# Kernel tuning notes

Measured on AMD Instinct MI355X. Metric: run time of the kernel, lower is better.

## Reference

```python
import jax, jax.numpy as jnp
import numpy as np

DIM = 1024
HEADS = 16
DH = DIM // HEADS          # 64
SEQ_LEN = 4096
LATENT = 1024
HIST = SEQ_LEN - LATENT    # 3072
LN_EPS = 1e-5


def setup_inputs() -> dict:
    key = jax.random.key(0)
    ks = jax.random.split(key, 5)
    b = 2
    x = jax.random.normal(ks[0], (b, SEQ_LEN, DIM), dtype=jnp.float32)
    s = 0.02
    Wq = jax.random.normal(ks[1], (DIM, DIM), dtype=jnp.float32) * s
    Wkv = jax.random.normal(ks[2], (DIM, DIM), dtype=jnp.float32) * s
    Wo = jax.random.normal(ks[3], (DIM, DIM), dtype=jnp.float32) * s
    bo = jnp.zeros((DIM,), dtype=jnp.float32)
    gamma = jnp.ones((DH,), dtype=jnp.float32)
    beta = jnp.zeros((DH,), dtype=jnp.float32)
    return {"x": x, "Wq": Wq, "Wkv": Wkv, "Wo": Wo, "bo": bo,
            "gamma": gamma, "beta": beta}


def _rotate_half(t):
    t1, t2 = jnp.split(t, 2, axis=-1)
    return jnp.concatenate([-t2, t1], axis=-1)


def reference(x, Wq, Wkv, Wo, bo, gamma, beta):
    b, n, dim = x.shape
    # projections (nn.Linear: y = x @ W.T), split heads -> (b, h, n, d)
    q = jnp.einsum('bnd,ed->bne', x, Wq).reshape(b, n, HEADS, DH).transpose(0, 2, 1, 3)
    kv = jnp.einsum('bnd,ed->bne', x, Wkv).reshape(b, n, HEADS, DH).transpose(0, 2, 1, 3)

    # layer_num == 0: queries only for the latent segment
    q = q[:, :, HIST:, :]  # (b, h, latent, d)

    # rotary embeddings: concat-style freqs over head dim
    inv_freq = 1.0 / (10000.0 ** (jnp.arange(0, DH, 2, dtype=jnp.float32) / DH))
    freqs = jnp.arange(n, dtype=jnp.float32)[:, None] * inv_freq[None, :]  # (n, DH/2)
    emb = jnp.concatenate([freqs, freqs], axis=-1)  # (n, DH)
    cos, sin = jnp.cos(emb), jnp.sin(emb)
    q = q * cos[HIST:] + _rotate_half(q) * sin[HIST:]
    kv = kv * cos + _rotate_half(kv) * sin

    q = q * (DH ** -0.5)

    # per-kv LayerNorm over head dim
    mu = kv.mean(axis=-1, keepdims=True)
    var = ((kv - mu) ** 2).mean(axis=-1, keepdims=True)
    kvn = (kv - mu) * jax.lax.rsqrt(var + LN_EPS) * gamma + beta

    attn = jnp.einsum('bhid,bhjd->bhij', q, kvn)  # (b, h, latent, n)

    # causal mask only on latent columns: col j (>= HIST) masked if j-HIST > i
    i = jnp.arange(LATENT)[:, None]
    j = jnp.arange(n)[None, :]
    mask = (j - HIST) > i  # false for history columns (j < HIST)
    neg = -jnp.finfo(attn.dtype).max
    attn = jnp.where(mask, neg, attn)

    attn = jax.nn.softmax(attn, axis=-1)
    out = jnp.einsum('bhij,bhjd->bhid', attn, kvn)  # (b, h, latent, d)
    out = out.transpose(0, 2, 1, 3).reshape(b, LATENT, dim)
    return jnp.einsum('bnd,ed->bne', out, Wo) + bo
```

## Files before the change

kernel.cpp:

```cpp
#include <hip/hip_runtime.h>
#include <hip/hip_bf16.h>
#include <cstdint>

#define DIMC 1024
#define HEADS 16
#define DHH 64
#define SEQ 4096
#define LATENT 1024
#define HISTC 3072
#define BATCH 2

typedef __attribute__((ext_vector_type(8))) __bf16 bf16x8;
typedef __attribute__((ext_vector_type(4))) float f32x4;
typedef __attribute__((ext_vector_type(16))) float f32x16;

__global__ void k_prep(const float* __restrict__ x, const float* __restrict__ Wq,
                       const float* __restrict__ Wkv, const float* __restrict__ Wo,
                       __bf16* __restrict__ x16, __bf16* __restrict__ wq16,
                       __bf16* __restrict__ wkv16, __bf16* __restrict__ wo16,
                       float2* __restrict__ cs) {
  int bidx = blockIdx.x;
  if (bidx < 2048) {
    int base = bidx * 256 + threadIdx.x;
#pragma unroll
// ... 76 lines not shown

#pragma unroll
  for (int m = 0; m < 4; ++m)
#pragma unroll
    for (int n = 0; n < 4; ++n)
#pragma unroll
      for (int r = 0; r < 4; ++r) {
        int row = m0 + wr * 64 + m * 16 + (l >> 4) * 4 + r;
        int col = n0 + wc * 64 + n * 16 + (l & 15);
        float v = acc[m][n][r];
        if (BIAS) v += bias[col];
        C[(size_t)row * N + col] = v;
      }
}

__launch_bounds__(256)
__global__ void k_gemmqkv(const __bf16* __restrict__ x16,
                          const __bf16* __restrict__ wkv16,
                          const __bf16* __restrict__ wq16,
                          __bf16* __restrict__ kvn, __bf16* __restrict__ kvnT,
                          __bf16* __restrict__ qb,
                          const float* __restrict__ gamma,
                          const float* __restrict__ beta,
                          const float2* __restrict__ cstab) {
  __shared__ __align__(16) char lds[16384];
  const int t = threadIdx.x, l = t & 63, w = t >> 6;
  const int wr = w >> 1, wc = w & 1;
  const int by = blockIdx.x % 80;
  const bool isq = by >= 64;
  const int m0 = (isq ? (by - 64) : by) * 128;
  const int n0 = (blockIdx.x / 80) * 128;
  const __bf16* Bw = isq ? wq16 : wkv16;
  const int lrow = l & 15, lk = l >> 4;
  f32x4 acc[4][4] = {};

  for (int k0 = 0; k0 < 1024; k0 += 32) {
    if (k0) __syncthreads();
#pragma unroll
    for (int i = 0; i < 2; ++i) {
      int c = i * 256 + t;
      int row = c >> 2, kc = c & 3;
      int mi = m0 + row;
      if (isq) mi += HISTC + (mi >> 10) * HISTC;
      gload16(lds + c * 16, x16 + (size_t)mi * 1024 + k0 + kc * 8);
      gload16(lds + 8192 + c * 16, Bw + (size_t)(n0 + row) * 1024 + k0 + kc * 8);
    }
    __syncthreads();
    bf16x8 af[4], bfr[4];
#pragma unroll
    for (int m = 0; m < 4; ++m)
      af[m] = *reinterpret_cast<const bf16x8*>(lds + (wr * 64 + m * 16 + lrow) * 64 + lk * 16);
#pragma unroll
    for (int n = 0; n < 4; ++n)
      bfr[n] = *reinterpret_cast<const bf16x8*>(lds + 8192 + (wc * 64 + n * 16 + lrow) * 64 + lk * 16);
#pragma unroll
    for (int m = 0; m < 4; ++m)
#pragma unroll
      for (int n = 0; n < 4; ++n)
        acc[m][n] = __builtin_amdgcn_mfma_f32_16x16x32_bf16(af[m], bfr[n], acc[m][n], 0, 0, 0);
  }

#pragma unroll
  for (int m = 0; m < 4; ++m)
#pragma unroll
    for (int r = 0; r < 4; ++r) {
      int rl = wr * 64 + m * 16 + lk * 4 + r;
      int pos = isq ? (HISTC + ((m0 + rl) & 1023)) : ((m0 + rl) & 4095);
      float2 cs0 = cstab[pos * 32 + lrow];
      float2 cs1 = cstab[pos * 32 + 16 + lrow];
      float a0 = acc[m][0][r], a2 = acc[m][2][r];
      acc[m][0][r] = a0 * cs0.x - a2 * cs0.y;
      acc[m][2][r] = a2 * cs0.x + a0 * cs0.y;
      float a1 = acc[m][1][r], a3 = acc[m][3][r];
      acc[m][1][r] = a1 * cs1.x - a3 * cs1.y;
      acc[m][3][r] = a3 * cs1.x + a1 * cs1.y;
    }

  const int h = (n0 + wc * 64) >> 6;
  if (!isq) {
    float g4[4], b4[4];
#pragma unroll
    for (int n = 0; n < 4; ++n) { g4[n] = gamma[n * 16 + lrow]; b4[n] = beta[n * 16 + lrow]; }
#pragma unroll
    for (int m = 0; m < 4; ++m)
#pragma unroll
      for (int r = 0; r < 4; ++r) {
        float s1 = acc[m][0][r] + acc[m][1][r] + acc[m][2][r] + acc[m][3][r];
        float s2 = acc[m][0][r] * acc[m][0][r] + acc[m][1][r] * acc[m][1][r] +
                   acc[m][2][r] * acc[m][2][r] + acc[m][3][r] * acc[m][3][r];
#pragma unroll
        for (int mk = 1; mk < 16; mk <<= 1) {
          s1 += __shfl_xor(s1, mk);
          s2 += __shfl_xor(s2, mk);
        }
        float mu = s1 * 0.015625f;
        float var = s2 * 0.015625f - mu * mu;
        float inv = rsqrtf(var + 1e-5f);
#pragma unroll
        for (int n = 0; n < 4; ++n)
          acc[m][n][r] = (acc[m][n][r] - mu) * inv * g4[n] + b4[n];
      }
    const size_t hb = (size_t)((m0 >> 12) * HEADS + h);
#pragma unroll
    for (int m = 0; m < 4; ++m)
#pragma unroll
      for (int r = 0; r < 4; ++r) {
        int pos = (m0 + wr * 64 + m * 16 + lk * 4 + r) & 4095;
#pragma unroll
        for (int n = 0; n < 4; ++n)
          kvn[(hb * SEQ + pos) * DHH + n * 16 + lrow] = (__bf16)acc[m][n][r];
      }
#pragma unroll
    for (int m = 0; m < 4; ++m) {
      int pos0 = (m0 + wr * 64 + m * 16 + lk * 4) & 4095;
      int sp = (pos0 & ~12) | ((pos0 & 4) << 1) | ((pos0 & 8) >> 1);
#pragma unroll
      for (int n = 0; n < 4; ++n) {
        union { __bf16 hh[4]; uint64_t u; } pk;
#pragma unroll
        for (int r = 0; r < 4; ++r) pk.hh[r] = (__bf16)acc[m][n][r];
        *reinterpret_cast<uint64_t*>(kvnT + (hb * DHH + n * 16 + lrow) * SEQ + sp) = pk.u;
      }
    }
  } else {
    const size_t hb = (size_t)((m0 >> 10) * HEADS + h);
#pragma unroll
    for (int m = 0; m < 4; ++m)
#pragma unroll
      for (int r = 0; r < 4; ++r) {
        int qi = (m0 + wr * 64 + m * 16 + lk * 4 + r) & 1023;
#pragma unroll
        for (int n = 0; n < 4; ++n)
          qb[(hb * LATENT + qi) * DHH + n * 16 + lrow] =
              (__bf16)(acc[m][n][r] * 0.18033688011112042f);
      }
  }
}

__device__ __forceinline__ float fexp2(float x) {
#if __has_builtin(__builtin_amdgcn_exp2f)
  return __builtin_amdgcn_exp2f(x);
#else
  return exp2f(x);
#endif
}

__device__ __forceinline__ unsigned pk2(float a, float b) {
  union { __bf16 h[2]; unsigned u; } x;
  x.h[0] = (__bf16)a; x.h[1] = (__bf16)b;
  return x.u;
}

__launch_bounds__(256)
__global__ void k_flash8(const __bf16* __restrict__ qb, const __bf16* __restrict__ kvn,
                         const __bf16* __restrict__ kvnT, float* __restrict__ part) {
  const int bid = blockIdx.x;
  const int grp = bid >> 9;
  const int jh = (bid >> 8) & 1;
  const int bh = (bid & 7) + 8 * grp;
  int itile = (bid >> 3) & 31;
  if (jh) itile = 31 - itile;
  const int h = bh & 15, b = bh >> 4;
  const int t = threadIdx.x, l = t & 63, w = t >> 6;
  const int q = l & 31, hi = l >> 5;
  const int iw = itile * 32;
  const int i = iw + q;
  const __bf16* qbase = qb + ((size_t)(b * HEADS + h) * LATENT + iw) * DHH;
  const __bf16* kbase = kvn + (size_t)(b * HEADS + h) * SEQ * DHH;
  const __bf16* vbase = kvnT + (size_t)(b * HEADS + h) * DHH * SEQ;

  __shared__ __align__(16) char smem[4][4352];
  __shared__ float Mlds[4][32];
  __shared__ float Llds[4][32];
  __bf16 (*Vw)[32] = reinterpret_cast<__bf16(*)[32]>(smem[w]);

  bf16x8 qf[4];
#pragma unroll
  for (int c = 0; c < 4; ++c)
    qf[c] = *reinterpret_cast<const bf16x8*>(qbase + (size_t)q * DHH + c * 16 + hi * 8);

  const f32x16 Z = {};
  f32x16 O0 = {}, O1 = {};
  float m_run = -INFINITY, lacc = 0.f;

  const int nt = itile + 97;
  const int s = jh * 4 + w;
  const int t0 = (nt * s) >> 3, t1 = (nt * (s + 1)) >> 3;

  const int srow = l >> 2, scol = l & 3;
  const int wchunk = (scol ^ (srow & 3)) * 8;
  const int sx = q & 3;
  bf16x8 vreg[4], kreg[4];
#pragma unroll
  for (int ii = 0; ii < 4; ++ii)
    vreg[ii] = *reinterpret_cast<const bf16x8*>(
        vbase + (size_t)(ii * 16 + srow) * SEQ + t0 * 32 + scol * 8);
#pragma unroll
  for (int c = 0; c < 4; ++c)
    kreg[c] = *reinterpret_cast<const bf16x8*>(
        kbase + (size_t)(t0 * 32 + q) * DHH + c * 16 + hi * 8);

  for (int tt = t0; tt < t1; ++tt) {
    const int j0 = tt * 32;
    f32x16 S = __builtin_amdgcn_mfma_f32_32x32x16_bf16(kreg[0], qf[0], Z, 0, 0, 0);
    S = __builtin_amdgcn_mfma_f32_32x32x16_bf16(kreg[1], qf[1], S, 0, 0, 0);
    S = __builtin_amdgcn_mfma_f32_32x32x16_bf16(kreg[2], qf[2], S, 0, 0, 0);
    S = __builtin_amdgcn_mfma_f32_32x32x16_bf16(kreg[3], qf[3], S, 0, 0, 0);
#pragma unroll
    for (int ii = 0; ii < 4; ++ii)
      *reinterpret_cast<bf16x8*>(&Vw[ii * 16 + srow][wchunk]) = vreg[ii];
    const int tn = (tt + 1 < t1) ? tt + 1 : tt;
#pragma unroll
    for (int ii = 0; ii < 4; ++ii)
      vreg[ii] = *reinterpret_cast<const bf16x8*>(
          vbase + (size_t)(ii * 16 + srow) * SEQ + tn * 32 + scol * 8);
#pragma unroll
    for (int c = 0; c < 4; ++c)
      kreg[c] = *reinterpret_cast<const bf16x8*>(
          kbase + (size_t)(tn * 32 + q) * DHH + c * 16 + hi * 8);
    if (j0 + 31 > iw + HISTC) {
#pragma unroll
      for (int r = 0; r < 16; ++r) {
        int j = j0 + (r & 3) + 8 * (r >> 2) + 4 * hi;
        if (j > i + HISTC) S[r] = -1e30f;
      }
    }
    float u1 = fmaxf(fmaxf(S[0], S[1]), S[2]);
    float u2 = fmaxf(fmaxf(S[3], S[4]), S[5]);
    float u3 = fmaxf(fmaxf(S[6], S[7]), S[8]);
    float u4 = fmaxf(fmaxf(S[9], S[10]), S[11]);
    float u5 = fmaxf(fmaxf(S[12], S[13]), S[14]);
    float pm = fmaxf(fmaxf(fmaxf(u1, u2), u3), fmaxf(fmaxf(u4, u5), S[15]));
    if (__any(pm > m_run + 8.0f)) {
      pm = fmaxf(pm, __shfl_xor(pm, 32));
      float mn = fmaxf(m_run, pm);
      float sc = fexp2(m_run - mn);
      m_run = mn;
      lacc *= sc;
#pragma unroll
      for (int r = 0; r < 16; ++r) { O0[r] *= sc; O1[r] *= sc; }
    }
    float p[16];
#pragma unroll
    for (int r = 0; r < 16; ++r) p[r] = fexp2(S[r] - m_run);
    float s8[8];
#pragma unroll
    for (int r = 0; r < 8; ++r) s8[r] = p[r] + p[r + 8];
    lacc += ((s8[0] + s8[4]) + (s8[1] + s8[5])) + ((s8[2] + s8[6]) + (s8[3] + s8[7]));
    union { unsigned u[4]; bf16x8 v; } pf0, pf1;
    pf0.u[0] = pk2(p[0], p[1]);   pf0.u[1] = pk2(p[2], p[3]);
    pf0.u[2] = pk2(p[4], p[5]);   pf0.u[3] = pk2(p[6], p[7]);
    pf1.u[0] = pk2(p[8], p[9]);   pf1.u[1] = pk2(p[10], p[11]);
    pf1.u[2] = pk2(p[12], p[13]); pf1.u[3] = pk2(p[14], p[15]);
    {
      bf16x8 va00 = *reinterpret_cast<const bf16x8*>(&Vw[q][(hi ^ sx) * 8]);
      bf16x8 va01 = *reinterpret_cast<const bf16x8*>(&Vw[q][((2 + hi) ^ sx) * 8]);
      bf16x8 va10 = *reinterpret_cast<const bf16x8*>(&Vw[32 + q][(hi ^ sx) * 8]);
      bf16x8 va11 = *reinterpret_cast<const bf16x8*>(&Vw[32 + q][((2 + hi) ^ sx) * 8]);
      O0 = __builtin_amdgcn_mfma_f32_32x32x16_bf16(va00, pf0.v, O0, 0, 0, 0);
      O0 = __builtin_amdgcn_mfma_f32_32x32x16_bf16(va01, pf1.v, O0, 0, 0, 0);
      O1 = __builtin_amdgcn_mfma_f32_32x32x16_bf16(va10, pf0.v, O1, 0, 0, 0);
      O1 = __builtin_amdgcn_mfma_f32_32x32x16_bf16(va11, pf1.v, O1, 0, 0, 0);
    }
  }
  float l_run = lacc + __shfl_xor(lacc, 32);

  const int pidx = (bh * 32 + itile) * 2 + jh;
  float* prow_base = part + (size_t)pidx * 32 * 68;
  float (*Ow)[33] = reinterpret_cast<float(*)[33]>(smem[w]);
  if (hi == 0) { Mlds[w][q] = m_run; Llds[w][q] = l_run; }
#pragma unroll
  for (int r = 0; r < 16; ++r)
    Ow[q][(r & 3) + 8 * (r >> 2) + 4 * hi] = O0[r];
  __syncthreads();
  const int mi = t >> 3, dl = (t & 7) * 4;
  float m0v = Mlds[0][mi], m1v = Mlds[1][mi], m2v = Mlds[2][mi], m3v = Mlds[3][mi];
  float mm = fmaxf(fmaxf(m0v, m1v), fmaxf(m2v, m3v));
  float sc0 = fexp2(m0v - mm), sc1 = fexp2(m1v - mm);
  float sc2 = fexp2(m2v - mm), sc3 = fexp2(m3v - mm);
  float ll = Llds[0][mi] * sc0 + Llds[1][mi] * sc1 + Llds[2][mi] * sc2 + Llds[3][mi] * sc3;
  float* prow = prow_base + (size_t)mi * 68;
  {
    float(*O0p)[33] = reinterpret_cast<float(*)[33]>(smem[0]);
    float(*O1p)[33] = reinterpret_cast<float(*)[33]>(smem[1]);
    float(*O2p)[33] = reinterpret_cast<float(*)[33]>(smem[2]);
    float(*O3p)[33] = reinterpret_cast<float(*)[33]>(smem[3]);
    float4 o;
    o.x = O0p[mi][dl + 0] * sc0 + O1p[mi][dl + 0] * sc1 + O2p[mi][dl + 0] * sc2 + O3p[mi][dl + 0] * sc3;
    o.y = O0p[mi][dl + 1] * sc0 + O1p[mi][dl + 1] * sc1 + O2p[mi][dl + 1] * sc2 + O3p[mi][dl + 1] * sc3;
    o.z = O0p[mi][dl + 2] * sc0 + O1p[mi][dl + 2] * sc1 + O2p[mi][dl + 2] * sc2 + O3p[mi][dl + 2] * sc3;
    o.w = O0p[mi][dl + 3] * sc0 + O1p[mi][dl + 3] * sc1 + O2p[mi][dl + 3] * sc2 + O3p[mi][dl + 3] * sc3;
    *reinterpret_cast<float4*>(prow + dl) = o;
    if ((t & 7) == 0) { prow[64] = mm; prow[65] = ll; }
  }
  __syncthreads();
#pragma unroll
  for (int r = 0; r < 16; ++r)
    Ow[q][(r & 3) + 8 * (r >> 2) + 4 * hi] = O1[r];
  __syncthreads();
  {
    float(*O0p)[33] = reinterpret_cast<float(*)[33]>(smem[0]);
    float(*O1p)[33] = reinterpret_cast<float(*)[33]>(smem[1]);
    float(*O2p)[33] = reinterpret_cast<float(*)[33]>(smem[2]);
    float(*O3p)[33] = reinterpret_cast<float(*)[33]>(smem[3]);
    float4 o;
    o.x = O0p[mi][dl + 0] * sc0 + O1p[mi][dl + 0] * sc1 + O2p[mi][dl + 0] * sc2 + O3p[mi][dl + 0] * sc3;
    o.y = O0p[mi][dl + 1] * sc0 + O1p[mi][dl + 1] * sc1 + O2p[mi][dl + 1] * sc2 + O3p[mi][dl + 1] * sc3;
    o.z = O0p[mi][dl + 2] * sc0 + O1p[mi][dl + 2] * sc1 + O2p[mi][dl + 2] * sc2 + O3p[mi][dl + 2] * sc3;
    o.w = O0p[mi][dl + 3] * sc0 + O1p[mi][dl + 3] * sc1 + O2p[mi][dl + 3] * sc2 + O3p[mi][dl + 3] * sc3;
    *reinterpret_cast<float4*>(prow + 32 + dl) = o;
  }
}

__global__ void k_fmerge(const float* __restrict__ part, __bf16* __restrict__ aout) {
  const int u = blockIdx.x;
  const int bh = u >> 5, itile = u & 31;
  const int b = bh >> 4, h = bh & 15, iw = itile * 32;
  const int t = threadIdx.x;
  const int mi = t >> 3, d0 = (t & 7) * 8;
  const float* p0 = part + ((size_t)(u * 2 + 0) * 32 + mi) * 68;
  const float* p1 = part + ((size_t)(u * 2 + 1) * 32 + mi) * 68;
  float m0 = p0[64], l0 = p0[65], m1 = p1[64], l1 = p1[65];
  float mm = fmaxf(m0, m1);
  float sc0 = fexp2(m0 - mm), sc1 = fexp2(m1 - mm);
  float inv = 1.f / (l0 * sc0 + l1 * sc1);
  union { __bf16 hh[8]; uint4 u4; } pk;
#pragma unroll
  for (int e = 0; e < 8; ++e)
    pk.hh[e] = (__bf16)((p0[d0 + e] * sc0 + p1[d0 + e] * sc1) * inv);
  *reinterpret_cast<uint4*>(aout + ((size_t)(b * LATENT) + iw + mi) * DIMC + h * DHH + d0) = pk.u4;
}

extern "C" void kernel_launch(void* const* d_in, const int* in_sizes, int n_in,
                              void* d_out, int out_size, void* d_ws, size_t ws_size,
                              hipStream_t stream) {
  const float* x = (const float*)d_in[0];
  const float* Wq = (const float*)d_in[1];
  const float* Wkv = (const float*)d_in[2];
  const float* Wo = (const float*)d_in[3];
  const float* bo = (const float*)d_in[4];
  const float* gamma = (const float*)d_in[5];
  const float* beta = (const float*)d_in[6];

  char* ws = (char*)d_ws;
  size_t o = 0;
  __bf16* x16 = (__bf16*)(ws + o);  o += (size_t)BATCH * SEQ * DIMC * 2;
  __bf16* wq16 = (__bf16*)(ws + o); o += (size_t)DIMC * DIMC * 2;
  __bf16* wkv16 = (__bf16*)(ws + o); o += (size_t)DIMC * DIMC * 2;
  __bf16* wo16 = (__bf16*)(ws + o); o += (size_t)DIMC * DIMC * 2;
  float2* cstab = (float2*)(ws + o); o += (size_t)SEQ * 32 * 8;
  __bf16* kvn = (__bf16*)(ws + o);  o += (size_t)BATCH * HEADS * SEQ * DHH * 2;
  __bf16* kvnT = (__bf16*)(ws + o); o += (size_t)BATCH * HEADS * SEQ * DHH * 2;
  __bf16* qb = (__bf16*)(ws + o);   o += (size_t)BATCH * HEADS * LATENT * DHH * 2;
  __bf16* aout = (__bf16*)(ws + o); o += (size_t)BATCH * LATENT * DIMC * 2;
  float* part = (float*)(ws + o);   o += (size_t)2048 * 32 * 68 * 4;

  k_prep<<<4096, 256, 0, stream>>>(x, Wq, Wkv, Wo, x16, wq16, wkv16, wo16, cstab);
  k_gemmqkv<<<640, 256, 0, stream>>>(x16, wkv16, wq16, kvn, kvnT, qb, gamma, beta, cstab);
  k_flash8<<<2048, 256, 0, stream>>>(qb, kvn, kvnT, part);
  k_fmerge<<<1024, 256, 0, stream>>>(part, aout);
  k_gemm<1><<<128, 256, 0, stream>>>(aout, wo16, (float*)d_out, bo, 2048, 1024, 1024);
}
```

Before: 175.8 us.

## Process 64 query rows per flash block and fold merge into kernel

Each flash-attention block now handles two 32-row query tiles that share every K and V tile loaded, so global and LDS traffic per query drops. The KV range of a tile is split across only the four waves of one block, so the cross-block partial buffer and the separate merge kernel go away and normalized bf16 output is written directly. The grid shrinks from 2048 to 512 blocks, which reduces parallelism, raises register pressure from four accumulators, and makes each wave's serial KV loop longer.

```diff
diff --git a/kernel.cpp b/kernel.cpp
--- a/kernel.cpp
+++ b/kernel.cpp
@@ -252,20 +252,19 @@
 }
 
 __launch_bounds__(256)
-__global__ void k_flash8(const __bf16* __restrict__ qb, const __bf16* __restrict__ kvn,
-                         const __bf16* __restrict__ kvnT, float* __restrict__ part) {
+__global__ void k_flash9(const __bf16* __restrict__ qb, const __bf16* __restrict__ kvn,
+                         const __bf16* __restrict__ kvnT, __bf16* __restrict__ aout) {
   const int bid = blockIdx.x;
-  const int grp = bid >> 9;
-  const int jh = (bid >> 8) & 1;
+  const int grp = bid >> 7;
   const int bh = (bid & 7) + 8 * grp;
-  int itile = (bid >> 3) & 31;
-  if (jh) itile = 31 - itile;
+  int itp = (bid >> 3) & 15;
+  if (grp >= 2) itp = 15 - itp;
   const int h = bh & 15, b = bh >> 4;
   const int t = threadIdx.x, l = t & 63, w = t >> 6;
   const int q = l & 31, hi = l >> 5;
-  const int iw = itile * 32;
-  const int i = iw + q;
-  const __bf16* qbase = qb + ((size_t)(b * HEADS + h) * LATENT + iw) * DHH;
+  const int iw0 = itp * 64;
+  const int i0 = iw0 + q, i1 = iw0 + 32 + q;
+  const __bf16* qbase = qb + ((size_t)(b * HEADS + h) * LATENT + iw0) * DHH;
   const __bf16* kbase = kvn + (size_t)(b * HEADS + h) * SEQ * DHH;
   const __bf16* vbase = kvnT + (size_t)(b * HEADS + h) * DHH * SEQ;
 
@@ -274,18 +273,20 @@
   __shared__ float Llds[4][32];
   __bf16 (*Vw)[32] = reinterpret_cast<__bf16(*)[32]>(smem[w]);
 
-  bf16x8 qf[4];
-#pragma unroll
-  for (int c = 0; c < 4; ++c)
-    qf[c] = *reinterpret_cast<const bf16x8*>(qbase + (size_t)q * DHH + c * 16 + hi * 8);
+  bf16x8 qf0[4], qf1[4];
+#pragma unroll
+  for (int c = 0; c < 4; ++c) {
+    qf0[c] = *reinterpret_cast<const bf16x8*>(qbase + (size_t)q * DHH + c * 16 + hi * 8);
+    qf1[c] = *reinterpret_cast<const bf16x8*>(qbase + (size_t)(32 + q) * DHH + c * 16 + hi * 8);
+  }
 
   const f32x16 Z = {};
-  f32x16 O0 = {}, O1 = {};
-  float m_run = -INFINITY, lacc = 0.f;
-
-  const int nt = itile + 97;
-  const int s = jh * 4 + w;
-  const int t0 = (nt * s) >> 3, t1 = (nt * (s + 1)) >> 3;
+  f32x16 O00 = {}, O01 = {}, O10 = {}, O11 = {};
+  float m0r = -INFINITY, lacc0 = 0.f;
+  float m1r = -INFINITY, lacc1 = 0.f;
+
+  const int nt = 2 * itp + 98;
+  const int t0 = (nt * w) >> 2, t1 = (nt * (w + 1)) >> 2;
 
   const int srow = l >> 2, scol = l & 3;
   const int wchunk = (scol ^ (srow & 3)) * 8;
@@ -302,10 +303,14 @@
 
   for (int tt = t0; tt < t1; ++tt) {
     const int j0 = tt * 32;
-    f32x16 S = __builtin_amdgcn_mfma_f32_32x32x16_bf16(kreg[0], qf[0], Z, 0, 0, 0);
-    S = __builtin_amdgcn_mfma_f32_32x32x16_bf16(kreg[1], qf[1], S, 0, 0, 0);
-    S = __builtin_amdgcn_mfma_f32_32x32x16_bf16(kreg[2], qf[2], S, 0, 0, 0);
-    S = __builtin_amdgcn_mfma_f32_32x32x16_bf16(kreg[3], qf[3], S, 0, 0, 0);
+    f32x16 S0 = __builtin_amdgcn_mfma_f32_32x32x16_bf16(kreg[0], qf0[0], Z, 0, 0, 0);
+    S0 = __builtin_amdgcn_mfma_f32_32x32x16_bf16(kreg[1], qf0[1], S0, 0, 0, 0);
+    S0 = __builtin_amdgcn_mfma_f32_32x32x16_bf16(kreg[2], qf0[2], S0, 0, 0, 0);
+    S0 = __builtin_amdgcn_mfma_f32_32x32x16_bf16(kreg[3], qf0[3], S0, 0, 0, 0);
+    f32x16 S1 = __builtin_amdgcn_mfma_f32_32x32x16_bf16(kreg[0], qf1[0], Z, 0, 0, 0);
+    S1 = __builtin_amdgcn_mfma_f32_32x32x16_bf16(kreg[1], qf1[1], S1, 0, 0, 0);
+    S1 = __builtin_amdgcn_mfma_f32_32x32x16_bf16(kreg[2], qf1[2], S1, 0, 0, 0);
+    S1 = __builtin_amdgcn_mfma_f32_32x32x16_bf16(kreg[3], qf1[3], S1, 0, 0, 0);
 #pragma unroll
     for (int ii = 0; ii < 4; ++ii)
       *reinterpret_cast<bf16x8*>(&Vw[ii * 16 + srow][wchunk]) = vreg[ii];
@@ -318,117 +323,189 @@
     for (int c = 0; c < 4; ++c)
       kreg[c] = *reinterpret_cast<const bf16x8*>(
           kbase + (size_t)(tn * 32 + q) * DHH + c * 16 + hi * 8);
-    if (j0 + 31 > iw + HISTC) {
+    bf16x8 va00 = *reinterpret_cast<const bf16x8*>(&Vw[q][(hi ^ sx) * 8]);
+    bf16x8 va01 = *reinterpret_cast<const bf16x8*>(&Vw[q][((2 + hi) ^ sx) * 8]);
+    bf16x8 va10 = *reinterpret_cast<const bf16x8*>(&Vw[32 + q][(hi ^ sx) * 8]);
+    bf16x8 va11 = *reinterpret_cast<const bf16x8*>(&Vw[32 + q][((2 + hi) ^ sx) * 8]);
+    if (j0 + 31 > i0 + HISTC - 31 + 31) {
 #pragma unroll
       for (int r = 0; r < 16; ++r) {
         int j = j0 + (r & 3) + 8 * (r >> 2) + 4 * hi;
-        if (j > i + HISTC) S[r] = -1e30f;
-      }
-    }
-    float u1 = fmaxf(fmaxf(S[0], S[1]), S[2]);
-    float u2 = fmaxf(fmaxf(S[3], S[4]), S[5]);
-    float u3 = fmaxf(fmaxf(S[6], S[7]), S[8]);
-    float u4 = fmaxf(fmaxf(S[9], S[10]), S[11]);
-    float u5 = fmaxf(fmaxf(S[12], S[13]), S[14]);
-    float pm = fmaxf(fmaxf(fmaxf(u1, u2), u3), fmaxf(fmaxf(u4, u5), S[15]));
-    if (__any(pm > m_run + 8.0f)) {
-      pm = fmaxf(pm, __shfl_xor(pm, 32));
-      float mn = fmaxf(m_run, pm);
-      float sc = fexp2(m_run - mn);
-      m_run = mn;
-      lacc *= sc;
-#pragma unroll
-      for (int r = 0; r < 16; ++r) { O0[r] *= sc; O1[r] *= sc; }
-    }
-    float p[16];
-#pragma unroll
-    for (int r = 0; r < 16; ++r) p[r] = fexp2(S[r] - m_run);
-    float s8[8];
-#pragma unroll
-    for (int r = 0; r < 8; ++r) s8[r] = p[r] + p[r + 8];
-    lacc += ((s8[0] + s8[4]) + (s8[1] + s8[5])) + ((s8[2] + s8[6]) + (s8[3] + s8[7]));
-    union { unsigned u[4]; bf16x8 v; } pf0, pf1;
-    pf0.u[0] = pk2(p[0], p[1]);   pf0.u[1] = pk2(p[2], p[3]);
-    pf0.u[2] = pk2(p[4], p[5]);   pf0.u[3] = pk2(p[6], p[7]);
-    pf1.u[0] = pk2(p[8], p[9]);   pf1.u[1] = pk2(p[10], p[11]);
-    pf1.u[2] = pk2(p[12], p[13]); pf1.u[3] = pk2(p[14], p[15]);
+        if (j > i0 + HISTC) S0[r] = -1e30f;
+      }
+    }
     {
-      bf16x8 va00 = *reinterpret_cast<const bf16x8*>(&Vw[q][(hi ^ sx) * 8]);
-      bf16x8 va01 = *reinterpret_cast<const bf16x8*>(&Vw[q][((2 + hi) ^ sx) * 8]);
-      bf16x8 va10 = *reinterpret_cast<const bf16x8*>(&Vw[32 + q][(hi ^ sx) * 8]);
-      bf16x8 va11 = *reinterpret_cast<const bf16x8*>(&Vw[32 + q][((2 + hi) ^ sx) * 8]);
-      O0 = __builtin_amdgcn_mfma_f32_32x32x16_bf16(va00, pf0.v, O0, 0, 0, 0);
-      O0 = __builtin_amdgcn_mfma_f32_32x32x16_bf16(va01, pf1.v, O0, 0, 0, 0);
-      O1 = __builtin_amdgcn_mfma_f32_32x32x16_bf16(va10, pf0.v, O1, 0, 0, 0);
-      O1 = __builtin_amdgcn_mfma_f32_32x32x16_bf16(va11, pf1.v, O1, 0, 0, 0);
-    }
-  }
-  float l_run = lacc + __shfl_xor(lacc, 32);
-
-  const int pidx = (bh * 32 + itile) * 2 + jh;
-  float* prow_base = part + (size_t)pidx * 32 * 68;
+      float u1 = fmaxf(fmaxf(S0[0], S0[1]), S0[2]);
+      float u2 = fmaxf(fmaxf(S0[3], S0[4]), S0[5]);
+      float u3 = fmaxf(fmaxf(S0[6], S0[7]), S0[8]);
+      float u4 = fmaxf(fmaxf(S0[9], S0[10]), S0[11]);
+      float u5 = fmaxf(fmaxf(S0[12], S0[13]), S0[14]);
+      float pm = fmaxf(fmaxf(fmaxf(u1, u2), u3), fmaxf(fmaxf(u4, u5), S0[15]));
+      if (__any(pm > m0r + 8.0f)) {
+        pm = fmaxf(pm, __shfl_xor(pm, 32));
+        float mn = fmaxf(m0r, pm);
+        float sc = fexp2(m0r - mn);
+        m0r = mn;
+        lacc0 *= sc;
+#pragma unroll
+        for (int r = 0; r < 16; ++r) { O00[r] *= sc; O01[r] *= sc; }
+      }
+      float p[16];
+#pragma unroll
+      for (int r = 0; r < 16; ++r) p[r] = fexp2(S0[r] - m0r);
+      float s8[8];
+#pragma unroll
+      for (int r = 0; r < 8; ++r) s8[r] = p[r] + p[r + 8];
+      lacc0 += ((s8[0] + s8[4]) + (s8[1] + s8[5])) + ((s8[2] + s8[6]) + (s8[3] + s8[7]));
+      union { unsigned u[4]; bf16x8 v; } pf0, pf1;
+      pf0.u[0] = pk2(p[0], p[1]);   pf0.u[1] = pk2(p[2], p[3]);
+      pf0.u[2] = pk2(p[4], p[5]);   pf0.u[3] = pk2(p[6], p[7]);
+      pf1.u[0] = pk2(p[8], p[9]);   pf1.u[1] = pk2(p[10], p[11]);
+      pf1.u[2] = pk2(p[12], p[13]); pf1.u[3] = pk2(p[14], p[15]);
+      O00 = __builtin_amdgcn_mfma_f32_32x32x16_bf16(va00, pf0.v, O00, 0, 0, 0);
+      O00 = __builtin_amdgcn_mfma_f32_32x32x16_bf16(va01, pf1.v, O00, 0, 0, 0);
+      O01 = __builtin_amdgcn_mfma_f32_32x32x16_bf16(va10, pf0.v, O01, 0, 0, 0);
+      O01 = __builtin_amdgcn_mfma_f32_32x32x16_bf16(va11, pf1.v, O01, 0, 0, 0);
+    }
+    if (j0 + 31 > iw0 + 32 + HISTC) {
+#pragma unroll
+      for (int r = 0; r < 16; ++r) {
+        int j = j0 + (r & 3) + 8 * (r >> 2) + 4 * hi;
+        if (j > i1 + HISTC) S1[r] = -1e30f;
+      }
+    }
+    {
+      float u1 = fmaxf(fmaxf(S1[0], S1[1]), S1[2]);
+      float u2 = fmaxf(fmaxf(S1[3], S1[4]), S1[5]);
+      float u3 = fmaxf(fmaxf(S1[6], S1[7]), S1[8]);
+      float u4 = fmaxf(fmaxf(S1[9], S1[10]), S1[11]);
+      float u5 = fmaxf(fmaxf(S1[12], S1[13]), S1[14]);
+      float pm = fmaxf(fmaxf(fmaxf(u1, u2), u3), fmaxf(fmaxf(u4, u5), S1[15]));
+      if (__any(pm > m1r + 8.0f)) {
+        pm = fmaxf(pm, __shfl_xor(pm, 32));
+        float mn = fmaxf(m1r, pm);
+        float sc = fexp2(m1r - mn);
+        m1r = mn;
+        lacc1 *= sc;
+#pragma unroll
+        for (int r = 0; r < 16; ++r) { O10[r] *= sc; O11[r] *= sc; }
+      }
+      float p[16];
+#pragma unroll
+      for (int r = 0; r < 16; ++r) p[r] = fexp2(S1[r] - m1r);
+      float s8[8];
+#pragma unroll
+      for (int r = 0; r < 8; ++r) s8[r] = p[r] + p[r + 8];
+      lacc1 += ((s8[0] + s8[4]) + (s8[1] + s8[5])) + ((s8[2] + s8[6]) + (s8[3] + s8[7]));
+      union { unsigned u[4]; bf16x8 v; } pf0, pf1;
+      pf0.u[0] = pk2(p[0], p[1]);   pf0.u[1] = pk2(p[2], p[3]);
+      pf0.u[2] = pk2(p[4], p[5]);   pf0.u[3] = pk2(p[6], p[7]);
+      pf1.u[0] = pk2(p[8], p[9]);   pf1.u[1] = pk2(p[10], p[11]);
+      pf1.u[2] = pk2(p[12], p[13]); pf1.u[3] = pk2(p[14], p[15]);
+      O10 = __builtin_amdgcn_mfma_f32_32x32x16_bf16(va00, pf0.v, O10, 0, 0, 0);
+      O10 = __builtin_amdgcn_mfma_f32_32x32x16_bf16(va01, pf1.v, O10, 0, 0, 0);
+      O11 = __builtin_amdgcn_mfma_f32_32x32x16_bf16(va10, pf0.v, O11, 0, 0, 0);
+      O11 = __builtin_amdgcn_mfma_f32_32x32x16_bf16(va11, pf1.v, O11, 0, 0, 0);
+    }
+  }
+  float l0r = lacc0 + __shfl_xor(lacc0, 32);
+  float l1r = lacc1 + __shfl_xor(lacc1, 32);
+
   float (*Ow)[33] = reinterpret_cast<float(*)[33]>(smem[w]);
-  if (hi == 0) { Mlds[w][q] = m_run; Llds[w][q] = l_run; }
+  const int mi = t >> 3, dl = (t & 7) * 4;
+  if (hi == 0) { Mlds[w][q] = m0r; Llds[w][q] = l0r; }
 #pragma unroll
   for (int r = 0; r < 16; ++r)
-    Ow[q][(r & 3) + 8 * (r >> 2) + 4 * hi] = O0[r];
-  __syncthreads();
-  const int mi = t >> 3, dl = (t & 7) * 4;
+    Ow[q][(r & 3) + 8 * (r >> 2) + 4 * hi] = O00[r];
+  __syncthreads();
   float m0v = Mlds[0][mi], m1v = Mlds[1][mi], m2v = Mlds[2][mi], m3v = Mlds[3][mi];
   float mm = fmaxf(fmaxf(m0v, m1v), fmaxf(m2v, m3v));
   float sc0 = fexp2(m0v - mm), sc1 = fexp2(m1v - mm);
   float sc2 = fexp2(m2v - mm), sc3 = fexp2(m3v - mm);
   float ll = Llds[0][mi] * sc0 + Llds[1][mi] * sc1 + Llds[2][mi] * sc2 + Llds[3][mi] * sc3;
-  float* prow = prow_base + (size_t)mi * 68;
+  float inv = 1.f / ll;
   {
-    float(*O0p)[33] = reinterpret_cast<float(*)[33]>(smem[0]);
-    float(*O1p)[33] = reinterpret_cast<float(*)[33]>(smem[1]);
-    float(*O2p)[33] = reinterpret_cast<float(*)[33]>(smem[2]);
-    float(*O3p)[33] = reinterpret_cast<float(*)[33]>(smem[3]);
-    float4 o;
-    o.x = O0p[mi][dl + 0] * sc0 + O1p[mi][dl + 0] * sc1 + O2p[mi][dl + 0] * sc2 + O3p[mi][dl + 0] * sc3;
-    o.y = O0p[mi][dl + 1] * sc0 + O1p[mi][dl + 1] * sc1 + O2p[mi][dl + 1] * sc2 + O3p[mi][dl + 1] * sc3;
-    o.z = O0p[mi][dl + 2] * sc0 + O1p[mi][dl + 2] * sc1 + O2p[mi][dl + 2] * sc2 + O3p[mi][dl + 2] * sc3;
-    o.w = O0p[mi][dl + 3] * sc0 + O1p[mi][dl + 3] * sc1 + O2p[mi][dl + 3] * sc2 + O3p[mi][dl + 3] * sc3;
-    *reinterpret_cast<float4*>(prow + dl) = o;
-    if ((t & 7) == 0) { prow[64] = mm; prow[65] = ll; }
+    float(*A0)[33] = reinterpret_cast<float(*)[33]>(smem[0]);
+    float(*A1)[33] = reinterpret_cast<float(*)[33]>(smem[1]);
+    float(*A2)[33] = reinterpret_cast<float(*)[33]>(smem[2]);
+    float(*A3)[33] = reinterpret_cast<float(*)[33]>(smem[3]);
+    __bf16* orow = aout + ((size_t)(b * LATENT) + iw0 + mi) * DIMC + h * DHH;
+    union { __bf16 hh[4]; uint2 u2; } pkv;
+#pragma unroll
+    for (int e = 0; e < 4; ++e) {
+      float o = A0[mi][dl + e] * sc0 + A1[mi][dl + e] * sc1 +
+                A2[mi][dl + e] * sc2 + A3[mi][dl + e] * sc3;
+      pkv.hh[e] = (__bf16)(o * inv);
+    }
+    *reinterpret_cast<uint2*>(orow + dl) = pkv.u2;
   }
   __syncthreads();
 #pragma unroll
   for (int r = 0; r < 16; ++r)
-    Ow[q][(r & 3) + 8 * (r >> 2) + 4 * hi] = O1[r];
+    Ow[q][(r & 3) + 8 * (r >> 2) + 4 * hi] = O01[r];
   __syncthreads();
   {
-    float(*O0p)[33] = reinterpret_cast<float(*)[33]>(smem[0]);
-    float(*O1p)[33] = reinterpret_cast<float(*)[33]>(smem[1]);
-    float(*O2p)[33] = reinterpret_cast<float(*)[33]>(smem[2]);
-    float(*O3p)[33] = reinterpret_cast<float(*)[33]>(smem[3]);
-    float4 o;
-    o.x = O0p[mi][dl + 0] * sc0 + O1p[mi][dl + 0] * sc1 + O2p[mi][dl + 0] * sc2 + O3p[mi][dl + 0] * sc3;
-    o.y = O0p[mi][dl + 1] * sc0 + O1p[mi][dl + 1] * sc1 + O2p[mi][dl + 1] * sc2 + O3p[mi][dl + 1] * sc3;
-    o.z = O0p[mi][dl + 2] * sc0 + O1p[mi][dl + 2] * sc1 + O2p[mi][dl + 2] * sc2 + O3p[mi][dl + 2] * sc3;
-    o.w = O0p[mi][dl + 3] * sc0 + O1p[mi][dl + 3] * sc1 + O2p[mi][dl + 3] * sc2 + O3p[mi][dl + 3] * sc3;
-    *reinterpret_cast<float4*>(prow + 32 + dl) = o;
-  }
-}
-
-__global__ void k_fmerge(const float* __restrict__ part, __bf16* __restrict__ aout) {
-  const int u = blockIdx.x;
-  const int bh = u >> 5, itile = u & 31;
-  const int b = bh >> 4, h = bh & 15, iw = itile * 32;
-  const int t = threadIdx.x;
-  const int mi = t >> 3, d0 = (t & 7) * 8;
-  const float* p0 = part + ((size_t)(u * 2 + 0) * 32 + mi) * 68;
-  const float* p1 = part + ((size_t)(u * 2 + 1) * 32 + mi) * 68;
-  float m0 = p0[64], l0 = p0[65], m1 = p1[64], l1 = p1[65];
-  float mm = fmaxf(m0, m1);
-  float sc0 = fexp2(m0 - mm), sc1 = fexp2(m1 - mm);
-  float inv = 1.f / (l0 * sc0 + l1 * sc1);
-  union { __bf16 hh[8]; uint4 u4; } pk;
-#pragma unroll
-  for (int e = 0; e < 8; ++e)
-    pk.hh[e] = (__bf16)((p0[d0 + e] * sc0 + p1[d0 + e] * sc1) * inv);
-  *reinterpret_cast<uint4*>(aout + ((size_t)(b * LATENT) + iw + mi) * DIMC + h * DHH + d0) = pk.u4;
+    float(*A0)[33] = reinterpret_cast<float(*)[33]>(smem[0]);
+    float(*A1)[33] = reinterpret_cast<float(*)[33]>(smem[1]);
+    float(*A2)[33] = reinterpret_cast<float(*)[33]>(smem[2]);
+    float(*A3)[33] = reinterpret_cast<float(*)[33]>(smem[3]);
+    __bf16* orow = aout + ((size_t)(b * LATENT) + iw0 + mi) * DIMC + h * DHH;
+    union { __bf16 hh[4]; uint2 u2; } pkv;
+#pragma unroll
+    for (int e = 0; e < 4; ++e) {
+      float o = A0[mi][dl + e] * sc0 + A1[mi][dl + e] * sc1 +
+                A2[mi][dl + e] * sc2 + A3[mi][dl + e] * sc3;
+      pkv.hh[e] = (__bf16)(o * inv);
+    }
+    *reinterpret_cast<uint2*>(orow + 32 + dl) = pkv.u2;
+  }
+  __syncthreads();
+  if (hi == 0) { Mlds[w][q] = m1r; Llds[w][q] = l1r; }
+#pragma unroll
+  for (int r = 0; r < 16; ++r)
+    Ow[q][(r & 3) + 8 * (r >> 2) + 4 * hi] = O10[r];
+  __syncthreads();
+  m0v = Mlds[0][mi]; m1v = Mlds[1][mi]; m2v = Mlds[2][mi]; m3v = Mlds[3][mi];
+  mm = fmaxf(fmaxf(m0v, m1v), fmaxf(m2v, m3v));
+  sc0 = fexp2(m0v - mm); sc1 = fexp2(m1v - mm);
+  sc2 = fexp2(m2v - mm); sc3 = fexp2(m3v - mm);
+  ll = Llds[0][mi] * sc0 + Llds[1][mi] * sc1 + Llds[2][mi] * sc2 + Llds[3][mi] * sc3;
+  inv = 1.f / ll;
+  {
+    float(*A0)[33] = reinterpret_cast<float(*)[33]>(smem[0]);
+    float(*A1)[33] = reinterpret_cast<float(*)[33]>(smem[1]);
+    float(*A2)[33] = reinterpret_cast<float(*)[33]>(smem[2]);
+    float(*A3)[33] = reinterpret_cast<float(*)[33]>(smem[3]);
+    __bf16* orow = aout + ((size_t)(b * LATENT) + iw0 + 32 + mi) * DIMC + h * DHH;
+    union { __bf16 hh[4]; uint2 u2; } pkv;
+#pragma unroll
+    for (int e = 0; e < 4; ++e) {
+      float o = A0[mi][dl + e] * sc0 + A1[mi][dl + e] * sc1 +
+                A2[mi][dl + e] * sc2 + A3[mi][dl + e] * sc3;
+      pkv.hh[e] = (__bf16)(o * inv);
+    }
+    *reinterpret_cast<uint2*>(orow + dl) = pkv.u2;
+  }
+  __syncthreads();
+#pragma unroll
+  for (int r = 0; r < 16; ++r)
+    Ow[q][(r & 3) + 8 * (r >> 2) + 4 * hi] = O11[r];
+  __syncthreads();
+  {
+    float(*A0)[33] = reinterpret_cast<float(*)[33]>(smem[0]);
+    float(*A1)[33] = reinterpret_cast<float(*)[33]>(smem[1]);
+    float(*A2)[33] = reinterpret_cast<float(*)[33]>(smem[2]);
+    float(*A3)[33] = reinterpret_cast<float(*)[33]>(smem[3]);
+    __bf16* orow = aout + ((size_t)(b * LATENT) + iw0 + 32 + mi) * DIMC + h * DHH;
+    union { __bf16 hh[4]; uint2 u2; } pkv;
+#pragma unroll
+    for (int e = 0; e < 4; ++e) {
+      float o = A0[mi][dl + e] * sc0 + A1[mi][dl + e] * sc1 +
+                A2[mi][dl + e] * sc2 + A3[mi][dl + e] * sc3;
+      pkv.hh[e] = (__bf16)(o * inv);
+    }
+    *reinterpret_cast<uint2*>(orow + 32 + dl) = pkv.u2;
+  }
 }
 
 extern "C" void kernel_launch(void* const* d_in, const int* in_sizes, int n_in,
@@ -453,11 +530,9 @@
   __bf16* kvnT = (__bf16*)(ws + o); o += (size_t)BATCH * HEADS * SEQ * DHH * 2;
   __bf16* qb = (__bf16*)(ws + o);   o += (size_t)BATCH * HEADS * LATENT * DHH * 2;
   __bf16* aout = (__bf16*)(ws + o); o += (size_t)BATCH * LATENT * DIMC * 2;
-  float* part = (float*)(ws + o);   o += (size_t)2048 * 32 * 68 * 4;
 
   k_prep<<<4096, 256, 0, stream>>>(x, Wq, Wkv, Wo, x16, wq16, wkv16, wo16, cstab);
   k_gemmqkv<<<640, 256, 0, stream>>>(x16, wkv16, wq16, kvn, kvnT, qb, gamma, beta, cstab);
-  k_flash8<<<2048, 256, 0, stream>>>(qb, kvn, kvnT, part);
-  k_fmerge<<<1024, 256, 0, stream>>>(part, aout);
+  k_flash9<<<512, 256, 0, stream>>>(qb, kvn, kvnT, aout);
   k_gemm<1><<<128, 256, 0, stream>>>(aout, wo16, (float*)d_out, bo, 2048, 1024, 1024);
 }
```

Result: faster. 159.5 us (-9.3%).

## Share K/V tiles across waves via double-buffered LDS in flash attention

Applied to the files above, without the earlier changes.

Each block now handles 128 query rows, one 32-row tile per wave. All four waves share each K/V tile, which is loaded into double-buffered LDS with async global-to-LDS copies, instead of each wave streaming its own KV split through registers. The KV range is split only two ways, so the in-block cross-wave merge goes away and each wave writes its partial state directly in MFMA layout for a simpler merge kernel. This cuts global K/V traffic by reusing each tile across waves, but adds a block barrier per tile, a 4x smaller grid (512 blocks), and causal-length imbalance between waves in the same block.

```diff
diff --git a/kernel.cpp b/kernel.cpp
--- a/kernel.cpp
+++ b/kernel.cpp
@@ -252,27 +252,31 @@
 }
 
 __launch_bounds__(256)
-__global__ void k_flash8(const __bf16* __restrict__ qb, const __bf16* __restrict__ kvn,
-                         const __bf16* __restrict__ kvnT, float* __restrict__ part) {
+__global__ void k_flash10(const __bf16* __restrict__ qb, const __bf16* __restrict__ kvn,
+                          const __bf16* __restrict__ kvnT, float* __restrict__ part) {
   const int bid = blockIdx.x;
-  const int grp = bid >> 9;
-  const int jh = (bid >> 8) & 1;
-  const int bh = (bid & 7) + 8 * grp;
-  int itile = (bid >> 3) & 31;
-  if (jh) itile = 31 - itile;
+  const int xcd = bid & 7;
+  const int u6 = bid >> 3;
+  const int jh = u6 & 1;
+  int itq = (u6 >> 1) & 7;
+  const int grpb = u6 >> 4;
+  if (grpb >= 2) itq = 7 - itq;
+  const int bh = xcd + 8 * grpb;
   const int h = bh & 15, b = bh >> 4;
   const int t = threadIdx.x, l = t & 63, w = t >> 6;
   const int q = l & 31, hi = l >> 5;
-  const int iw = itile * 32;
-  const int i = iw + q;
-  const __bf16* qbase = qb + ((size_t)(b * HEADS + h) * LATENT + iw) * DHH;
+  const int iw0 = itq * 128;
+  const int iwv = iw0 + w * 32;
+  const int i = iwv + q;
+  const __bf16* qbase = qb + ((size_t)(b * HEADS + h) * LATENT + iwv) * DHH;
   const __bf16* kbase = kvn + (size_t)(b * HEADS + h) * SEQ * DHH;
   const __bf16* vbase = kvnT + (size_t)(b * HEADS + h) * DHH * SEQ;
 
-  __shared__ __align__(16) char smem[4][4352];
-  __shared__ float Mlds[4][32];
-  __shared__ float Llds[4][32];
-  __bf16 (*Vw)[32] = reinterpret_cast<__bf16(*)[32]>(smem[w]);
+  __shared__ __align__(16) __bf16 Kl[2][32][64];
+  __shared__ __align__(16) __bf16 Vl[2][64][32];
+
+  const int krow = t >> 3, kgc = ((t & 7) ^ (krow & 7)) * 8;
+  const int vrow = t >> 2, vgc = ((t & 3) ^ (vrow & 3)) * 8;
 
   bf16x8 qf[4];
 #pragma unroll
@@ -283,42 +287,36 @@
   f32x16 O0 = {}, O1 = {};
   float m_run = -INFINITY, lacc = 0.f;
 
-  const int nt = itile + 97;
-  const int s = jh * 4 + w;
-  const int t0 = (nt * s) >> 3, t1 = (nt * (s + 1)) >> 3;
-
-  const int srow = l >> 2, scol = l & 3;
-  const int wchunk = (scol ^ (srow & 3)) * 8;
+  const int nt = 4 * itq + 100;
+  const int t0 = (nt * jh) >> 1, t1 = (nt * (jh + 1)) >> 1;
   const int sx = q & 3;
-  bf16x8 vreg[4], kreg[4];
-#pragma unroll
-  for (int ii = 0; ii < 4; ++ii)
-    vreg[ii] = *reinterpret_cast<const bf16x8*>(
-        vbase + (size_t)(ii * 16 + srow) * SEQ + t0 * 32 + scol * 8);
-#pragma unroll
-  for (int c = 0; c < 4; ++c)
-    kreg[c] = *reinterpret_cast<const bf16x8*>(
-        kbase + (size_t)(t0 * 32 + q) * DHH + c * 16 + hi * 8);
+
+  {
+    const int j0 = t0 * 32;
+    gload16((char*)&Kl[0][0][0] + t * 16, kbase + (size_t)(j0 + krow) * DHH + kgc);
+    gload16((char*)&Vl[0][0][0] + t * 16, vbase + (size_t)vrow * SEQ + j0 + vgc);
+  }
+  __syncthreads();
 
   for (int tt = t0; tt < t1; ++tt) {
+    const int cur = (tt - t0) & 1;
     const int j0 = tt * 32;
-    f32x16 S = __builtin_amdgcn_mfma_f32_32x32x16_bf16(kreg[0], qf[0], Z, 0, 0, 0);
-    S = __builtin_amdgcn_mfma_f32_32x32x16_bf16(kreg[1], qf[1], S, 0, 0, 0);
-    S = __builtin_amdgcn_mfma_f32_32x32x16_bf16(kreg[2], qf[2], S, 0, 0, 0);
-    S = __builtin_amdgcn_mfma_f32_32x32x16_bf16(kreg[3], qf[3], S, 0, 0, 0);
-#pragma unroll
-    for (int ii = 0; ii < 4; ++ii)
-      *reinterpret_cast<bf16x8*>(&Vw[ii * 16 + srow][wchunk]) = vreg[ii];
-    const int tn = (tt + 1 < t1) ? tt + 1 : tt;
-#pragma unroll
-    for (int ii = 0; ii < 4; ++ii)
-      vreg[ii] = *reinterpret_cast<const bf16x8*>(
-          vbase + (size_t)(ii * 16 + srow) * SEQ + tn * 32 + scol * 8);
-#pragma unroll
-    for (int c = 0; c < 4; ++c)
-      kreg[c] = *reinterpret_cast<const bf16x8*>(
-          kbase + (size_t)(tn * 32 + q) * DHH + c * 16 + hi * 8);
-    if (j0 + 31 > iw + HISTC) {
+    const char* Kb = (const char*)&Kl[cur][0][0];
+    const char* Vb = (const char*)&Vl[cur][0][0];
+    bf16x8 kf0 = *reinterpret_cast<const bf16x8*>(Kb + q * 128 + ((0 + hi) ^ (q & 7)) * 16);
+    bf16x8 kf1 = *reinterpret_cast<const bf16x8*>(Kb + q * 128 + ((2 + hi) ^ (q & 7)) * 16);
+    bf16x8 kf2 = *reinterpret_cast<const bf16x8*>(Kb + q * 128 + ((4 + hi) ^ (q & 7)) * 16);
+    bf16x8 kf3 = *reinterpret_cast<const bf16x8*>(Kb + q * 128 + ((6 + hi) ^ (q & 7)) * 16);
+    f32x16 S = __builtin_amdgcn_mfma_f32_32x32x16_bf16(kf0, qf[0], Z, 0, 0, 0);
+    S = __builtin_amdgcn_mfma_f32_32x32x16_bf16(kf1, qf[1], S, 0, 0, 0);
+    S = __builtin_amdgcn_mfma_f32_32x32x16_bf16(kf2, qf[2], S, 0, 0, 0);
+    S = __builtin_amdgcn_mfma_f32_32x32x16_bf16(kf3, qf[3], S, 0, 0, 0);
+    if (tt + 1 < t1) {
+      const int j0n = (tt + 1) * 32;
+      gload16((char*)&Kl[cur ^ 1][0][0] + t * 16, kbase + (size_t)(j0n + krow) * DHH + kgc);
+      gload16((char*)&Vl[cur ^ 1][0][0] + t * 16, vbase + (size_t)vrow * SEQ + j0n + vgc);
+    }
+    if (j0 + 31 > iwv + HISTC) {
 #pragma unroll
       for (int r = 0; r < 16; ++r) {
         int j = j0 + (r & 3) + 8 * (r >> 2) + 4 * hi;
@@ -353,82 +351,58 @@
     pf1.u[0] = pk2(p[8], p[9]);   pf1.u[1] = pk2(p[10], p[11]);
     pf1.u[2] = pk2(p[12], p[13]); pf1.u[3] = pk2(p[14], p[15]);
     {
-      bf16x8 va00 = *reinterpret_cast<const bf16x8*>(&Vw[q][(hi ^ sx) * 8]);
-      bf16x8 va01 = *reinterpret_cast<const bf16x8*>(&Vw[q][((2 + hi) ^ sx) * 8]);
-      bf16x8 va10 = *reinterpret_cast<const bf16x8*>(&Vw[32 + q][(hi ^ sx) * 8]);
-      bf16x8 va11 = *reinterpret_cast<const bf16x8*>(&Vw[32 + q][((2 + hi) ^ sx) * 8]);
+      bf16x8 va00 = *reinterpret_cast<const bf16x8*>(Vb + q * 64 + (hi ^ sx) * 16);
+      bf16x8 va01 = *reinterpret_cast<const bf16x8*>(Vb + q * 64 + ((2 + hi) ^ sx) * 16);
+      bf16x8 va10 = *reinterpret_cast<const bf16x8*>(Vb + (32 + q) * 64 + (hi ^ sx) * 16);
+      bf16x8 va11 = *reinterpret_cast<const bf16x8*>(Vb + (32 + q) * 64 + ((2 + hi) ^ sx) * 16);
       O0 = __builtin_amdgcn_mfma_f32_32x32x16_bf16(va00, pf0.v, O0, 0, 0, 0);
       O0 = __builtin_amdgcn_mfma_f32_32x32x16_bf16(va01, pf1.v, O0, 0, 0, 0);
       O1 = __builtin_amdgcn_mfma_f32_32x32x16_bf16(va10, pf0.v, O1, 0, 0, 0);
       O1 = __builtin_amdgcn_mfma_f32_32x32x16_bf16(va11, pf1.v, O1, 0, 0, 0);
     }
+    __syncthreads();
   }
   float l_run = lacc + __shfl_xor(lacc, 32);
 
-  const int pidx = (bh * 32 + itile) * 2 + jh;
-  float* prow_base = part + (size_t)pidx * 32 * 68;
-  float (*Ow)[33] = reinterpret_cast<float(*)[33]>(smem[w]);
-  if (hi == 0) { Mlds[w][q] = m_run; Llds[w][q] = l_run; }
-#pragma unroll
-  for (int r = 0; r < 16; ++r)
-    Ow[q][(r & 3) + 8 * (r >> 2) + 4 * hi] = O0[r];
-  __syncthreads();
-  const int mi = t >> 3, dl = (t & 7) * 4;
-  float m0v = Mlds[0][mi], m1v = Mlds[1][mi], m2v = Mlds[2][mi], m3v = Mlds[3][mi];
-  float mm = fmaxf(fmaxf(m0v, m1v), fmaxf(m2v, m3v));
-  float sc0 = fexp2(m0v - mm), sc1 = fexp2(m1v - mm);
-  float sc2 = fexp2(m2v - mm), sc3 = fexp2(m3v - mm);
-  float ll = Llds[0][mi] * sc0 + Llds[1][mi] * sc1 + Llds[2][mi] * sc2 + Llds[3][mi] * sc3;
-  float* prow = prow_base + (size_t)mi * 68;
-  {
-    float(*O0p)[33] = reinterpret_cast<float(*)[33]>(smem[0]);
-    float(*O1p)[33] = reinterpret_cast<float(*)[33]>(smem[1]);
-    float(*O2p)[33] = reinterpret_cast<float(*)[33]>(smem[2]);
-    float(*O3p)[33] = reinterpret_cast<float(*)[33]>(smem[3]);
-    float4 o;
-    o.x = O0p[mi][dl + 0] * sc0 + O1p[mi][dl + 0] * sc1 + O2p[mi][dl + 0] * sc2 + O3p[mi][dl + 0] * sc3;
-    o.y = O0p[mi][dl + 1] * sc0 + O1p[mi][dl + 1] * sc1 + O2p[mi][dl + 1] * sc2 + O3p[mi][dl + 1] * sc3;
-    o.z = O0p[mi][dl + 2] * sc0 + O1p[mi][dl + 2] * sc1 + O2p[mi][dl + 2] * sc2 + O3p[mi][dl + 2] * sc3;
-    o.w = O0p[mi][dl + 3] * sc0 + O1p[mi][dl + 3] * sc1 + O2p[mi][dl + 3] * sc2 + O3p[mi][dl + 3] * sc3;
-    *reinterpret_cast<float4*>(prow + dl) = o;
-    if ((t & 7) == 0) { prow[64] = mm; prow[65] = ll; }
-  }
-  __syncthreads();
-#pragma unroll
-  for (int r = 0; r < 16; ++r)
-    Ow[q][(r & 3) + 8 * (r >> 2) + 4 * hi] = O1[r];
-  __syncthreads();
-  {
-    float(*O0p)[33] = reinterpret_cast<float(*)[33]>(smem[0]);
-    float(*O1p)[33] = reinterpret_cast<float(*)[33]>(smem[1]);
-    float(*O2p)[33] = reinterpret_cast<float(*)[33]>(smem[2]);
-    float(*O3p)[33] = reinterpret_cast<float(*)[33]>(smem[3]);
-    float4 o;
-    o.x = O0p[mi][dl + 0] * sc0 + O1p[mi][dl + 0] * sc1 + O2p[mi][dl + 0] * sc2 + O3p[mi][dl + 0] * sc3;
-    o.y = O0p[mi][dl + 1] * sc0 + O1p[mi][dl + 1] * sc1 + O2p[mi][dl + 1] * sc2 + O3p[mi][dl + 1] * sc3;
-    o.z = O0p[mi][dl + 2] * sc0 + O1p[mi][dl + 2] * sc1 + O2p[mi][dl + 2] * sc2 + O3p[mi][dl + 2] * sc3;
-    o.w = O0p[mi][dl + 3] * sc0 + O1p[mi][dl + 3] * sc1 + O2p[mi][dl + 3] * sc2 + O3p[mi][dl + 3] * sc3;
-    *reinterpret_cast<float4*>(prow + 32 + dl) = o;
-  }
-}
-
-__global__ void k_fmerge(const float* __restrict__ part, __bf16* __restrict__ aout) {
+  const int pidx = (bh * 8 + itq) * 2 + jh;
+  float* pw = part + (size_t)(pidx * 4 + w) * 34 * 64;
+#pragma unroll
+  for (int r = 0; r < 16; ++r) pw[r * 64 + l] = O0[r];
+#pragma unroll
+  for (int r = 0; r < 16; ++r) pw[(16 + r) * 64 + l] = O1[r];
+  pw[32 * 64 + l] = m_run;
+  pw[33 * 64 + l] = l_run;
+}
+
+__global__ void k_fmerge10(const float* __restrict__ part, __bf16* __restrict__ aout) {
   const int u = blockIdx.x;
-  const int bh = u >> 5, itile = u & 31;
-  const int b = bh >> 4, h = bh & 15, iw = itile * 32;
+  const int bh = u >> 3, itq = u & 7;
+  const int b = bh >> 4, h = bh & 15;
   const int t = threadIdx.x;
-  const int mi = t >> 3, d0 = (t & 7) * 8;
-  const float* p0 = part + ((size_t)(u * 2 + 0) * 32 + mi) * 68;
-  const float* p1 = part + ((size_t)(u * 2 + 1) * 32 + mi) * 68;
-  float m0 = p0[64], l0 = p0[65], m1 = p1[64], l1 = p1[65];
+  const int w = t >> 6, sub = t & 63, q = sub & 31, hi = sub >> 5;
+  const float* pa = part + (size_t)((u * 2 + 0) * 4 + w) * 34 * 64;
+  const float* pb = part + (size_t)((u * 2 + 1) * 4 + w) * 34 * 64;
+  float m0 = pa[32 * 64 + sub], l0 = pa[33 * 64 + sub];
+  float m1 = pb[32 * 64 + sub], l1 = pb[33 * 64 + sub];
   float mm = fmaxf(m0, m1);
   float sc0 = fexp2(m0 - mm), sc1 = fexp2(m1 - mm);
   float inv = 1.f / (l0 * sc0 + l1 * sc1);
-  union { __bf16 hh[8]; uint4 u4; } pk;
-#pragma unroll
-  for (int e = 0; e < 8; ++e)
-    pk.hh[e] = (__bf16)((p0[d0 + e] * sc0 + p1[d0 + e] * sc1) * inv);
-  *reinterpret_cast<uint4*>(aout + ((size_t)(b * LATENT) + iw + mi) * DIMC + h * DHH + d0) = pk.u4;
+  const int row = itq * 128 + w * 32 + q;
+  __bf16* orow = aout + ((size_t)(b * LATENT) + row) * DIMC + h * DHH;
+#pragma unroll
+  for (int g = 0; g < 4; ++g) {
+    union { __bf16 hh[4]; uint2 u2; } pk;
+#pragma unroll
+    for (int e = 0; e < 4; ++e)
+      pk.hh[e] = (__bf16)((pa[(4 * g + e) * 64 + sub] * sc0 +
+                           pb[(4 * g + e) * 64 + sub] * sc1) * inv);
+    *reinterpret_cast<uint2*>(orow + 8 * g + 4 * hi) = pk.u2;
+#pragma unroll
+    for (int e = 0; e < 4; ++e)
+      pk.hh[e] = (__bf16)((pa[(16 + 4 * g + e) * 64 + sub] * sc0 +
+                           pb[(16 + 4 * g + e) * 64 + sub] * sc1) * inv);
+    *reinterpret_cast<uint2*>(orow + 32 + 8 * g + 4 * hi) = pk.u2;
+  }
 }
 
 extern "C" void kernel_launch(void* const* d_in, const int* in_sizes, int n_in,
@@ -453,11 +427,11 @@
   __bf16* kvnT = (__bf16*)(ws + o); o += (size_t)BATCH * HEADS * SEQ * DHH * 2;
   __bf16* qb = (__bf16*)(ws + o);   o += (size_t)BATCH * HEADS * LATENT * DHH * 2;
   __bf16* aout = (__bf16*)(ws + o); o += (size_t)BATCH * LATENT * DIMC * 2;
-  float* part = (float*)(ws + o);   o += (size_t)2048 * 32 * 68 * 4;
+  float* part = (float*)(ws + o);   o += (size_t)512 * 4 * 34 * 64 * 4;
 
   k_prep<<<4096, 256, 0, stream>>>(x, Wq, Wkv, Wo, x16, wq16, wkv16, wo16, cstab);
   k_gemmqkv<<<640, 256, 0, stream>>>(x16, wkv16, wq16, kvn, kvnT, qb, gamma, beta, cstab);
-  k_flash8<<<2048, 256, 0, stream>>>(qb, kvn, kvnT, part);
-  k_fmerge<<<1024, 256, 0, stream>>>(part, aout);
+  k_flash10<<<512, 256, 0, stream>>>(qb, kvn, kvnT, part);
+  k_fmerge10<<<256, 256, 0, stream>>>(part, aout);
   k_gemm<1><<<128, 256, 0, stream>>>(aout, wo16, (float*)d_out, bo, 2048, 1024, 1024);
 }
```

New measurement: 157.3 us. 1.12x faster.
